# Optimization experiments

Hardware: AMD Instinct MI355X
Metric: run time of the kernel (lower is better)

Reference implementation:

```python
import jax, jax.numpy as jnp
import numpy as np

PI = 3.1415927410125732
N = 4096
L = 1.28e-3          # box side [m]
VEL = 5e-7
RC = 3.15e-6         # Rc = diameter/2
RR = 8e-6
RO = 2.5e-5
RA = np.inf
DT_TRANS = 1.4e-14   # DT (translational diffusion)
DR = 0.0028
GAMMA = 25.0
DT = 0.2             # timestep dt
COLL_ITERS = 30      # fixed cap for collision-resolution do-while (orig caps at 1000)


def setup_inputs() -> dict:
    key = jax.random.key(0)
    ks = jax.random.split(key, 7)
    pos_re = jax.random.uniform(ks[0], (N,), jnp.float32) * L
    pos_im = jax.random.uniform(ks[1], (N,), jnp.float32) * L
    ang = jax.random.uniform(ks[2], (N,), jnp.float32, -PI, PI)
    ori_re = jnp.cos(ang)
    ori_im = jnp.sin(ang)
    deltas = jax.random.uniform(ks[3], (N,), jnp.float32) * 0.5
    rot_noise = jax.random.normal(ks[4], (N,), jnp.float32)
    tn_re = jax.random.normal(ks[5], (N,), jnp.float32)
    tn_im = jax.random.normal(ks[6], (N,), jnp.float32)
    return {"pos_re": pos_re, "pos_im": pos_im, "ori_re": ori_re, "ori_im": ori_im,
            "deltas": deltas, "rot_noise": rot_noise, "tn_re": tn_re, "tn_im": tn_im}


def _wrap(diff):
    # torch get_anglediff wrap: (-2pi,2pi) -> ~(-pi,pi)
    diff = jnp.where(diff <= -PI, jnp.mod(diff, PI), diff)
    return diff - (diff >= PI).astype(diff.dtype) * (2.0 * PI)


def _anglediff(a, b):
    return _wrap(jnp.angle(a) - jnp.angle(b))


def _cossim(a, b):
    # nn.CosineSimilarity(dim=1, eps=1e-14) on view_as_real vectors
    dot = a.real * b.real + a.imag * b.imag
    na = jnp.maximum(jnp.abs(a), 1e-14)
    nb = jnp.maximum(jnp.abs(b), 1e-14)
    return dot / (na * nb)


def _mvc(W, z):
    # real [n,n] mask @ complex [n] vector
    return W @ z.real + 1j * (W @ z.imag)


def _solve_collisions(pos):
    n = pos.shape[0]
    eye_f = jnp.eye(n, dtype=jnp.float32)
    eye_c = eye_f.astype(pos.dtype)

    def step(p):
        diff = p[None, :] - p[:, None] + eye_c  # [i,j] = pos_j - pos_i; diag dummy 1 (nan-safe)
        absd = jnp.abs(diff)
        coll = absd <= (2.0 * RC - eye_f)       # diag threshold negative -> self excluded
        move = jnp.where(coll, diff / jnp.where(coll, absd, 1.0) * ((2.1 * RC - absd) * 0.5), 0.0)
        return p - move.sum(axis=1), coll.sum()

    def body(carry, _):
        p, cont = carry
        p_new, ncoll = step(p)
        p = jnp.where(cont, p_new, p)           # do-while: apply move, then continue if collisions
        return (p, jnp.logical_and(cont, ncoll > 0)), None

    body = jax.checkpoint(body)
    (pos, _), _ = jax.lax.scan(body, (pos, jnp.array(True)), None, length=COLL_ITERS)
    return pos


def _forward(pos_re, pos_im, ori_re, ori_im, deltas, rot_noise, tn_re, tn_im):
    pos = (pos_re + 1j * pos_im).astype(jnp.complex64)
    ori = (ori_re + 1j * ori_im).astype(jnp.complex64)
    n = pos.shape[0]
    eye_b = jnp.eye(n, dtype=bool)

    # pairwise |pos_i - pos_j|; diag made 1 to keep abs() grad-safe (diag is masked out / re-added below)
    dists = jnp.abs(pos[:, None] - pos[None, :] + jnp.eye(n, dtype=pos.dtype))
    mask_rr = (dists <= RR) & ~eye_b              # repulsion zone, self excluded (eye subtracted in orig)
    mask_ro = (dists <= RO + RC) | eye_b          # orientation zone, self included (diag dist 0 in orig)
    mask_ra = (dists <= RA + RC) | eye_b          # Ra = inf -> all ones

    # alpha == 2*pi exactly -> within_view branch skipped (matches original)
    ang = jnp.angle(ori)
    abs_ad = jnp.abs(_wrap(ang[:, None] - ang[None, :]))
    in_front = abs_ad < PI / 2

    Wrr = (mask_rr & in_front).astype(jnp.float32)
    Wro = mask_ro.astype(jnp.float32)
    Wra = mask_ra.astype(jnp.float32)

    n_r = Wrr.sum(axis=1)
    S = _mvc(Wrr, pos) / jnp.maximum(n_r, 1.0) - pos * jnp.sign(n_r)
    d = -S

    n_a = Wra.sum(axis=1)
    cms = _mvc(Wra, pos) / jnp.maximum(n_a, 1.0)
    Ps = cms - pos * jnp.sign(n_a)

    osum = _mvc(Wro, ori)
    left = Ps * jnp.exp(1j * deltas)
    right = Ps * jnp.exp(-1j * deltas)

    # T (=300) >= T_release (=200): choose best turn by cosine similarity
    best = jnp.where(_cossim(left, osum) >= _cossim(right, osum), left, right)

    has_rep = jnp.abs(d) > 0.0
    d_safe = jnp.where(has_rep, d, jnp.ones_like(d))
    att = jnp.where(has_rep, _anglediff(d_safe, ori), _anglediff(best, ori))

    s2dr = np.float32(np.sqrt(2.0 * DR))
    sdt = np.float32(np.sqrt(DT))
    rot = jnp.exp(1j * (DT * GAMMA * DR * jnp.sin(att) + rot_noise * s2dr * sdt))

    # complex standard normal: real/imag each N(0, 1/sqrt(2))
    tnoise = (tn_re + 1j * tn_im) * np.float32(np.sqrt(0.5)) * np.float32(np.sqrt(2.0 * DT_TRANS))
    trans = DT * VEL * ori + tnoise * sdt

    new_pos = _solve_collisions(pos + trans)
    new_ori = ori * rot

    c2r = lambda z: jnp.stack([z.real, z.imag], axis=-1)
    # [5, N, 2]: positions, orientations, orientation_sums, leftturns, rightturns (real views)
    return jnp.stack([c2r(new_pos), c2r(new_ori), c2r(osum), c2r(left), c2r(right)], axis=0)


def reference(pos_re, pos_im, ori_re, ori_im, deltas, rot_noise, tn_re, tn_im):
    return _forward(pos_re, pos_im, ori_re, ori_im, deltas, rot_noise, tn_re, tn_im)
```

## Files before the change

### kernel.cpp

```cpp
#include <hip/hip_runtime.h>

#define NPART 4096
#define PI_F 3.1415927410125732f
#define TWO_PI_F 6.2831854820251465f
#define NBCAP 14336
#define SENT 4096

__device__ __forceinline__ float wrapf(float d) {
    if (d <= -PI_F) {
        d = fmodf(d, PI_F);
        if (d < 0.0f) d += PI_F;
    }
    if (d >= PI_F) d -= TWO_PI_F;
    return d;
}

__global__ __launch_bounds__(512)
void k_interact(const float* __restrict__ pr, const float* __restrict__ pim,
                const float* __restrict__ orr, const float* __restrict__ oim,
                const float* __restrict__ deltas,
                const float* __restrict__ rot_noise,
                const float* __restrict__ tn_re, const float* __restrict__ tn_im,
                float* __restrict__ out,
                float2* __restrict__ recPos, int* __restrict__ recMeta,
                unsigned short* __restrict__ recNbr, int* __restrict__ gcnt) {
    constexpr float RR_F  = 8e-6f;
    constexpr float RR2   = RR_F * RR_F;
    constexpr float ROC_F = (float)(2.5e-5 + 3.15e-6);
    constexpr float ROC2  = ROC_F * ROC_F;
    constexpr float CUT_F = 14.3e-6f;
    constexpr float CUT2  = CUT_F * CUT_F;

    __shared__ float2 lsP[512];
    __shared__ float2 lsO[512];
    __shared__ float rA0[512], rA1[512], rA2[512], rA3[512], rA4[512];
    __shared__ float rB0[512], rB1[512], rB2[512], rB3[512], rB4[512];
    __shared__ float cr_[512], ci_[512];
    __shared__ int ncnt[16];
    __shared__ unsigned short nbrL[16 * 16];

    int tid = threadIdx.x;
    int li = tid & 7, sl = tid >> 3;
    int i0 = blockIdx.x * 16 + li;
    int i1 = i0 + 8;

    if (tid < 16) ncnt[tid] = 0;

    float pxA = pr[i0], pyA = pim[i0], oxA = orr[i0], oyA = oim[i0];
    float pxB = pr[i1], pyB = pim[i1], oxB = orr[i1], oyB = oim[i1];

    float nAr = 0.0f, SAre = 0.0f, SAim = 0.0f, oAre = 0.0f, oAim = 0.0f;
    float nBr = 0.0f, SBre = 0.0f, SBim = 0.0f, oBre = 0.0f, oBim = 0.0f;
    float cs_re = 0.0f, cs_im = 0.0f;

    for (int c = 0; c < 8; ++c) {
        int j0 = c * 512;
        __syncthreads();
        float jr = pr[j0 + tid], ji = pim[j0 + tid];
        lsP[tid] = make_float2(jr, ji);
        lsO[tid] = make_float2(orr[j0 + tid], oim[j0 + tid]);
        cs_re += jr; cs_im += ji;
        __syncthreads();
#pragma unroll
        for (int t = 0; t < 8; ++t) {
            int jj = sl * 8 + ((t + sl) & 7);
            int j = j0 + jj;
            float2 pv = lsP[jj];
            float drA = pxA - pv.x, diA = pyA - pv.y;
            float d2A = drA * drA + diA * diA;
            float drB = pxB - pv.x, diB = pyB - pv.y;
            float d2B = drB * drB + diB * diB;
            if (__any((d2A <= ROC2) | (d2B <= ROC2))) {
                float2 ov = lsO[jj];
                if (d2A <= ROC2) { oAre += ov.x; oAim += ov.y; }
                float dotA = oxA * ov.x + oyA * ov.y;
                if ((d2A <= RR2) & (dotA > 0.0f) & (j != i0)) {
                    nAr += 1.0f; SAre += pv.x; SAim += pv.y;
                }
                if (d2A <= CUT2 && j != i0) {
                    int slot = atomicAdd(&ncnt[li], 1);
                    if (slot < 16) nbrL[li * 16 + slot] = (unsigned short)j;
                }
                if (d2B <= ROC2) { oBre += ov.x; oBim += ov.y; }
                float dotB = oxB * ov.x + oyB * ov.y;
                if ((d2B <= RR2) & (dotB > 0.0f) & (j != i1)) {
                    nBr += 1.0f; SBre += pv.x; SBim += pv.y;
                }
                if (d2B <= CUT2 && j != i1) {
                    int slot = atomicAdd(&ncnt[li + 8], 1);
                    if (slot < 16) nbrL[(li + 8) * 16 + slot] = (unsigned short)j;
                }
            }
        }
    }

    rA0[tid] = nAr; rA1[tid] = SAre; rA2[tid] = SAim; rA3[tid] = oAre; rA4[tid] = oAim;
    rB0[tid] = nBr; rB1[tid] = SBre; rB2[tid] = SBim; rB3[tid] = oBre; rB4[tid] = oBim;
    cr_[tid] = cs_re; ci_[tid] = cs_im;
    __syncthreads();
    for (int s = 256; s >= 8; s >>= 1) {
        if (tid < s) {
            rA0[tid] += rA0[tid + s]; rA1[tid] += rA1[tid + s];
            rA2[tid] += rA2[tid + s]; rA3[tid] += rA3[tid + s];
            rA4[tid] += rA4[tid + s];
            rB0[tid] += rB0[tid + s]; rB1[tid] += rB1[tid + s];
            rB2[tid] += rB2[tid + s]; rB3[tid] += rB3[tid + s];
            rB4[tid] += rB4[tid + s];
            cr_[tid] += cr_[tid + s];  ci_[tid] += ci_[tid + s];
        }
        __syncthreads();
    }
    if (tid < 4) { cr_[tid] += cr_[tid + 4]; ci_[tid] += ci_[tid + 4]; }
    __syncthreads();
    if (tid < 2) { cr_[tid] += cr_[tid + 2]; ci_[tid] += ci_[tid + 2]; }
    __syncthreads();
    if (tid == 0) { cr_[0] += cr_[1]; ci_[0] += ci_[1]; }
    __syncthreads();

    if (tid < 16) {
        int i = blockIdx.x * 16 + tid;
        float n_r, S_re, S_im, o_re, o_im, px, py, ox, oy;
        if (tid < 8) {
            n_r = rA0[tid]; S_re = rA1[tid]; S_im = rA2[tid];
            o_re = rA3[tid]; o_im = rA4[tid];
            px = pxA; py = pyA; ox = oxA; oy = oyA;
        } else {
            int g = tid - 8;
            n_r = rB0[g]; S_re = rB1[g]; S_im = rB2[g];
            o_re = rB3[g]; o_im = rB4[g];
            px = pxB; py = pyB; ox = oxB; oy = oyB;
        }

        float maxnr = fmaxf(n_r, 1.0f);
        float sgn = (n_r > 0.0f) ? 1.0f : 0.0f;
        float Sre = S_re / maxnr - px * sgn;
        float Sim = S_im / maxnr - py * sgn;
        float d_re = -Sre, d_im = -Sim;

        float cmsx = cr_[0] * (1.0f / 4096.0f);
        float cmsy = ci_[0] * (1.0f / 4096.0f);
        float Ps_re = cmsx - px;
        float Ps_im = cmsy - py;

        float dl = deltas[i];
        float cd = cosf(dl), sd = sinf(dl);
        float l_re = Ps_re * cd - Ps_im * sd;
        float l_im = Ps_re * sd + Ps_im * cd;
        float r_re = Ps_re * cd + Ps_im * sd;
        float r_im = Ps_im * cd - Ps_re * sd;

        float nb   = fmaxf(hypotf(o_re, o_im), 1e-14f);
        float na_l = fmaxf(hypotf(l_re, l_im), 1e-14f);
        float na_r = fmaxf(hypotf(r_re, r_im), 1e-14f);
        float csl = (l_re * o_re + l_im * o_im) / (na_l * nb);
        float csr = (r_re * o_re + r_im * o_im) / (na_r * nb);
        float b_re = (csl >= csr) ? l_re : r_re;
        float b_im = (csl >= csr) ? l_im : r_im;

        float ai = atan2f(oy, ox);
        bool has_rep = (d_re != 0.0f) || (d_im != 0.0f);
        float att;
        if (has_rep) att = wrapf(atan2f(d_im, d_re) - ai);
        else         att = wrapf(atan2f(b_im, b_re) - ai);

        constexpr float GDD  = (float)(0.2 * 25.0 * 0.0028);
        constexpr float S2DR = 0.07483314773547883f;
        constexpr float SDT  = 0.44721359549995793f;
        float theta = GDD * sinf(att) + (rot_noise[i] * S2DR) * SDT;
        float rr_ = cosf(theta), ri_ = sinf(theta);

        float no_re = ox * rr_ - oy * ri_;
        float no_im = ox * ri_ + oy * rr_;

        constexpr float DTVEL = (float)(0.2 * 5e-7);
        constexpr float C1 = 0.70710678118654752f;
        constexpr float C2 = 1.6733200530681511e-07f;
        float t_re = DTVEL * ox + ((tn_re[i] * C1) * C2) * SDT;
        float t_im = DTVEL * oy + ((tn_im[i] * C1) * C2) * SDT;
        float p0x = px + t_re, p0y = py + t_im;

        float2* o2 = (float2*)out;
        o2[i]            = make_float2(p0x, p0y);
        o2[1 * 4096 + i] = make_float2(no_re, no_im);
        o2[2 * 4096 + i] = make_float2(o_re, o_im);
        o2[3 * 4096 + i] = make_float2(l_re, l_im);
        o2[4 * 4096 + i] = make_float2(r_re, r_im);

        int c = min(ncnt[tid], 16);
        if (c > 0) {
            int cp = (c + 3) & ~3;
            int slot = atomicAdd(&gcnt[0], 1);
            int eoff = atomicAdd(&gcnt[1], cp);
            if (eoff + cp <= NBCAP) {
                recPos[slot] = make_float2(p0x, p0y);
                recMeta[slot] = i | (c << 12) | (eoff << 17);
                for (int m = 0; m < cp; ++m)
                    recNbr[eoff + m] = (m < c) ? nbrL[tid * 16 + m]
                                               : (unsigned short)SENT;
            } else {
                recPos[slot] = make_float2(p0x, p0y);
                recMeta[slot] = i;
            }
        }
    }
}

__global__ __launch_bounds__(1024)
void k_coll_all(const float2* __restrict__ recPos, const int* __restrict__ recMeta,
                const unsigned short* __restrict__ recNbr,
                const int* __restrict__ gcnt, float* __restrict__ out) {
    constexpr float TWO_RC  = (float)(2.0 * 3.15e-6);
    constexpr float TWO_RC2 = TWO_RC * TWO_RC;
    constexpr float C21RC   = (float)(2.1 * 3.15e-6);

    __shared__ float2 pos[NPART + 2];
    __shared__ __align__(16) unsigned short nbr[NBCAP];
    __shared__ int flg[2];

    int tid = threadIdx.x;
    int n = gcnt[0];
    int totE = min(gcnt[1], NBCAP);

    int nU4 = (totE + 7) >> 3;
    const uint4* src4 = (const uint4*)recNbr;
    uint4* dst4 = (uint4*)nbr;
    for (int e = tid; e < nU4; e += 1024) dst4[e] = src4[e];

    if (tid == 0) {
        pos[SENT] = make_float2(1e9f, 1e9f);
        flg[0] = 0; flg[1] = 0;
    }

    float myx[4], myy[4];
    int myi[4], myc[4], myo[4];
#pragma unroll
    for (int s = 0; s < 4; ++s) {
        int slot = s * 1024 + tid;
        myc[s] = 0; myi[s] = SENT; myo[s] = 0;
        if (slot < n) {
            float2 p = recPos[slot];
            int meta = recMeta[slot];
            myx[s] = p.x; myy[s] = p.y;
            myi[s] = meta & 4095;
            myc[s] = (meta >> 12) & 31;
            myo[s] = (unsigned)meta >> 17;
            pos[myi[s]] = p;
        }
    }
    __syncthreads();

    int nq0[4], nq1[4], nq2[4], nq3[4];
#pragma unroll
    for (int s = 0; s < 4; ++s) {
        nq0[s] = SENT; nq1[s] = SENT; nq2[s] = SENT; nq3[s] = SENT;
        if (myc[s] > 0) {
            uint2 w = *(const uint2*)&nbr[myo[s]];
            nq0[s] = w.x & 0xffff; nq1[s] = w.x >> 16;
            nq2[s] = w.y & 0xffff; nq3[s] = w.y >> 16;
        }
    }

    for (int it = 0; it < 30; ++it) {
        float nx[4], ny[4];
        int ncs[4];
#pragma unroll
        for (int s = 0; s < 4; ++s) {
            ncs[s] = 0;
            int c = myc[s];
            if (c > 0) {
                float px = myx[s], py = myy[s];
                float mre = 0.0f, mim = 0.0f;
                int nc = 0;
                float2 q0 = pos[nq0[s]], q1 = pos[nq1[s]];
                float2 q2 = pos[nq2[s]], q3 = pos[nq3[s]];
#define COLL_ONE(q)                                                     \
                {                                                       \
                    float dr = (q).x - px, di = (q).y - py;             \
                    float d2 = dr * dr + di * di;                       \
                    if (d2 <= TWO_RC2) {                                \
                        float a = sqrtf(d2);                            \
                        float mm = (C21RC - a) * 0.5f / a;              \
                        mre += dr * mm; mim += di * mm; ++nc;           \
                    }                                                   \
                }
                COLL_ONE(q0) COLL_ONE(q1) COLL_ONE(q2) COLL_ONE(q3)
                for (int m0 = 4; m0 < c; m0 += 4) {
                    uint2 w = *(const uint2*)&nbr[myo[s] + m0];
                    int j0 = w.x & 0xffff, j1 = w.x >> 16;
                    int j2 = w.y & 0xffff, j3 = w.y >> 16;
                    float2 t0 = pos[j0], t1 = pos[j1], t2 = pos[j2], t3 = pos[j3];
                    COLL_ONE(t0) COLL_ONE(t1) COLL_ONE(t2) COLL_ONE(t3)
                }
#undef COLL_ONE
                ncs[s] = nc;
                nx[s] = px - mre; ny[s] = py - mim;
            }
        }
        __syncthreads();
#pragma unroll
        for (int s = 0; s < 4; ++s) {
            if (ncs[s] > 0) {
                myx[s] = nx[s]; myy[s] = ny[s];
                pos[myi[s]] = make_float2(nx[s], ny[s]);
            }
        }
        int any = ncs[0] | ncs[1] | ncs[2] | ncs[3];
        if (any) flg[it & 1] = 1;
        if (tid == 0) flg[(it + 1) & 1] = 0;
        __syncthreads();
        if (flg[it & 1] == 0) break;
    }

    float2* o2 = (float2*)out;
#pragma unroll
    for (int s = 0; s < 4; ++s)
        if (s * 1024 + tid < n) o2[myi[s]] = make_float2(myx[s], myy[s]);
}

extern "C" void kernel_launch(void* const* d_in, const int* in_sizes, int n_in,
                              void* d_out, int out_size, void* d_ws, size_t ws_size,
                              hipStream_t stream) {
    const float* pos_re = (const float*)d_in[0];
    const float* pos_im = (const float*)d_in[1];
    const float* ori_re = (const float*)d_in[2];
    const float* ori_im = (const float*)d_in[3];
    const float* deltas = (const float*)d_in[4];
    const float* rot_noise = (const float*)d_in[5];
    const float* tn_re = (const float*)d_in[6];
    const float* tn_im = (const float*)d_in[7];
    float* out = (float*)d_out;

    int* gcnt = (int*)d_ws;
    float2* recPos = (float2*)((char*)d_ws + 16);
    int* recMeta   = (int*)(recPos + NPART);
    unsigned short* recNbr = (unsigned short*)(recMeta + NPART);

    hipMemsetAsync(gcnt, 0, 16, stream);
    k_interact<<<256, 512, 0, stream>>>(pos_re, pos_im, ori_re, ori_im,
                                        deltas, rot_noise, tn_re, tn_im,
                                        out, recPos, recMeta, recNbr, gcnt);
    k_coll_all<<<1, 1024, 0, stream>>>(recPos, recMeta, recNbr, gcnt, out);
}
```

Before: 116.7 us.

## Skip collision checks for particles whose neighbours did not move

Adds a per-particle shared-memory stamp recording the last iteration each particle moved. A particle only recomputes its collision sum if it moved itself or one of its neighbours moved in the previous iteration. The neighbour list is no longer staged into shared memory and is read from global memory instead, which removes the upfront copy but makes the tail-neighbour reads slower. The change also guards the first four neighbour loads by count. Together these aim to cut redundant iterations of distance work, at the cost of extra stamp lookups and global reads.

```diff
diff --git a/kernel.cpp b/kernel.cpp
--- a/kernel.cpp
+++ b/kernel.cpp
@@ -214,18 +214,13 @@
     constexpr float C21RC   = (float)(2.1 * 3.15e-6);
 
     __shared__ float2 pos[NPART + 2];
-    __shared__ __align__(16) unsigned short nbr[NBCAP];
+    __shared__ unsigned short stamp[NPART + 2];
     __shared__ int flg[2];
 
     int tid = threadIdx.x;
     int n = gcnt[0];
-    int totE = min(gcnt[1], NBCAP);
-
-    int nU4 = (totE + 7) >> 3;
-    const uint4* src4 = (const uint4*)recNbr;
-    uint4* dst4 = (uint4*)nbr;
-    for (int e = tid; e < nU4; e += 1024) dst4[e] = src4[e];
-
+
+    for (int k = tid; k < NPART + 2; k += 1024) stamp[k] = 0xFFFFu;
     if (tid == 0) {
         pos[SENT] = make_float2(1e9f, 1e9f);
         flg[0] = 0; flg[1] = 0;
@@ -233,10 +228,14 @@
 
     float myx[4], myy[4];
     int myi[4], myc[4], myo[4];
+    int nq0[4], nq1[4], nq2[4], nq3[4];
+    bool mvd[4];
 #pragma unroll
     for (int s = 0; s < 4; ++s) {
         int slot = s * 1024 + tid;
         myc[s] = 0; myi[s] = SENT; myo[s] = 0;
+        nq0[s] = SENT; nq1[s] = SENT; nq2[s] = SENT; nq3[s] = SENT;
+        mvd[s] = false;
         if (slot < n) {
             float2 p = recPos[slot];
             int meta = recMeta[slot];
@@ -245,21 +244,16 @@
             myc[s] = (meta >> 12) & 31;
             myo[s] = (unsigned)meta >> 17;
             pos[myi[s]] = p;
-        }
-    }
-    __syncthreads();
-
-    int nq0[4], nq1[4], nq2[4], nq3[4];
-#pragma unroll
-    for (int s = 0; s < 4; ++s) {
-        nq0[s] = SENT; nq1[s] = SENT; nq2[s] = SENT; nq3[s] = SENT;
-        if (myc[s] > 0) {
-            uint2 w = *(const uint2*)&nbr[myo[s]];
-            nq0[s] = w.x & 0xffff; nq1[s] = w.x >> 16;
-            nq2[s] = w.y & 0xffff; nq3[s] = w.y >> 16;
-        }
-    }
-
+            if (myc[s] > 0) {
+                uint2 w = *(const uint2*)&recNbr[myo[s]];
+                nq0[s] = w.x & 0xffff; nq1[s] = w.x >> 16;
+                nq2[s] = w.y & 0xffff; nq3[s] = w.y >> 16;
+            }
+        }
+    }
+    __syncthreads();
+
+    const float2 FARP = make_float2(1e9f, 1e9f);
     for (int it = 0; it < 30; ++it) {
         float nx[4], ny[4];
         int ncs[4];
@@ -267,44 +261,64 @@
         for (int s = 0; s < 4; ++s) {
             ncs[s] = 0;
             int c = myc[s];
-            if (c > 0) {
-                float px = myx[s], py = myy[s];
-                float mre = 0.0f, mim = 0.0f;
-                int nc = 0;
-                float2 q0 = pos[nq0[s]], q1 = pos[nq1[s]];
-                float2 q2 = pos[nq2[s]], q3 = pos[nq3[s]];
+            if (c <= 0) continue;
+            bool chk = (it == 0) || mvd[s];
+            if (!chk) {
+                unsigned last = (unsigned)(it - 1);
+                chk = (stamp[nq0[s]] == last);
+                if (c > 1) chk |= (stamp[nq1[s]] == last);
+                if (c > 2) chk |= (stamp[nq2[s]] == last);
+                if (c > 3) chk |= (stamp[nq3[s]] == last);
+                for (int m0 = 4; m0 < c && !chk; m0 += 4) {
+                    uint2 w = *(const uint2*)&recNbr[myo[s] + m0];
+                    chk |= (stamp[w.x & 0xffff] == last);
+                    if (m0 + 1 < c) chk |= (stamp[w.x >> 16] == last);
+                    if (m0 + 2 < c) chk |= (stamp[w.y & 0xffff] == last);
+                    if (m0 + 3 < c) chk |= (stamp[w.y >> 16] == last);
+                }
+            }
+            if (!chk) continue;
+            float px = myx[s], py = myy[s];
+            float mre = 0.0f, mim = 0.0f;
+            int nc = 0;
+            float2 q0 = pos[nq0[s]];
+            float2 q1 = (c > 1) ? pos[nq1[s]] : FARP;
+            float2 q2 = (c > 2) ? pos[nq2[s]] : FARP;
+            float2 q3 = (c > 3) ? pos[nq3[s]] : FARP;
 #define COLL_ONE(q)                                                     \
-                {                                                       \
-                    float dr = (q).x - px, di = (q).y - py;             \
-                    float d2 = dr * dr + di * di;                       \
-                    if (d2 <= TWO_RC2) {                                \
-                        float a = sqrtf(d2);                            \
-                        float mm = (C21RC - a) * 0.5f / a;              \
-                        mre += dr * mm; mim += di * mm; ++nc;           \
-                    }                                                   \
-                }
-                COLL_ONE(q0) COLL_ONE(q1) COLL_ONE(q2) COLL_ONE(q3)
-                for (int m0 = 4; m0 < c; m0 += 4) {
-                    uint2 w = *(const uint2*)&nbr[myo[s] + m0];
-                    int j0 = w.x & 0xffff, j1 = w.x >> 16;
-                    int j2 = w.y & 0xffff, j3 = w.y >> 16;
-                    float2 t0 = pos[j0], t1 = pos[j1], t2 = pos[j2], t3 = pos[j3];
-                    COLL_ONE(t0) COLL_ONE(t1) COLL_ONE(t2) COLL_ONE(t3)
-                }
+            {                                                           \
+                float dr = (q).x - px, di = (q).y - py;                 \
+                float d2 = dr * dr + di * di;                           \
+                if (d2 <= TWO_RC2) {                                    \
+                    float a = sqrtf(d2);                                \
+                    float mm = (C21RC - a) * 0.5f / a;                  \
+                    mre += dr * mm; mim += di * mm; ++nc;               \
+                }                                                       \
+            }
+            COLL_ONE(q0) COLL_ONE(q1) COLL_ONE(q2) COLL_ONE(q3)
+            for (int m0 = 4; m0 < c; m0 += 4) {
+                uint2 w = *(const uint2*)&recNbr[myo[s] + m0];
+                int j0 = w.x & 0xffff, j1 = w.x >> 16;
+                int j2 = w.y & 0xffff, j3 = w.y >> 16;
+                float2 t0 = pos[j0], t1 = pos[j1], t2 = pos[j2], t3 = pos[j3];
+                COLL_ONE(t0) COLL_ONE(t1) COLL_ONE(t2) COLL_ONE(t3)
+            }
 #undef COLL_ONE
-                ncs[s] = nc;
-                nx[s] = px - mre; ny[s] = py - mim;
-            }
-        }
-        __syncthreads();
+            ncs[s] = nc;
+            nx[s] = px - mre; ny[s] = py - mim;
+        }
+        __syncthreads();
+        int any = 0;
 #pragma unroll
         for (int s = 0; s < 4; ++s) {
+            mvd[s] = (ncs[s] > 0);
             if (ncs[s] > 0) {
                 myx[s] = nx[s]; myy[s] = ny[s];
                 pos[myi[s]] = make_float2(nx[s], ny[s]);
-            }
-        }
-        int any = ncs[0] | ncs[1] | ncs[2] | ncs[3];
+                stamp[myi[s]] = (unsigned short)it;
+                any = 1;
+            }
+        }
         if (any) flg[it & 1] = 1;
         if (tid == 0) flg[(it + 1) & 1] = 0;
         __syncthreads();
```

Measured after the change: 124.2 us. +6.4%, slower.
